# Performance work log

Measured on AMD Instinct MI355X. Metric: run time of the kernel, lower is better.

Reference implementation:

```python
import jax, jax.numpy as jnp
import numpy as np
from jax import lax

B, T, E, D = 32, 4096, 512, 512     # batch, x_steps, eunits, dunits
A, C, F = 128, 32, 15               # attn_dim, conv_channel, aconv_filts
K = 2 * F + 1                       # location conv kernel size
NEG = -1e9


def setup_inputs() -> dict:
    key = jax.random.key(0)
    ks = jax.random.split(key, 12)
    value = jax.random.normal(ks[0], (B, T, E), dtype=jnp.float32)
    value_length = jax.random.randint(ks[1], (B,), T // 2, T + 1).astype(jnp.int32)
    query = jax.random.normal(ks[2], (B, D), dtype=jnp.float32)
    # dirac initialization per initialize_weights()
    prev_attn_weight = jax.nn.one_hot(jnp.zeros((B,), jnp.int32), T, dtype=jnp.float32)
    accum_attn_weight = prev_attn_weight
    s = 0.02
    Wv = jax.random.normal(ks[3], (E, A), dtype=jnp.float32) * s
    bv = jnp.zeros((A,), jnp.float32)
    Wq = jax.random.normal(ks[4], (D, A), dtype=jnp.float32) * s
    conv_k = jax.random.normal(ks[5], (K, 1, C), dtype=jnp.float32) * s  # WIO
    Wl = jax.random.normal(ks[6], (C, A), dtype=jnp.float32) * s
    att_v = jax.random.normal(ks[7], (A,), dtype=jnp.float32)
    att_g = jnp.asarray(np.sqrt(1.0 / A), jnp.float32)
    att_b = jnp.zeros((A,), jnp.float32)
    score_bias = jnp.asarray(0.0, jnp.float32)
    return {"value": value, "value_length": value_length, "query": query,
            "accum_attn_weight": accum_attn_weight, "prev_attn_weight": prev_attn_weight,
            "Wv": Wv, "bv": bv, "Wq": Wq, "conv_k": conv_k, "Wl": Wl,
            "att_v": att_v, "att_g": att_g, "att_b": att_b, "score_bias": score_bias}


def _forward(value, value_length, query, accum_attn_weight, prev_attn_weight,
             Wv, bv, Wq, conv_k, Wl, att_v, att_g, att_b, score_bias):
    # projections
    densed_value = value @ Wv + bv                      # [B,T,A]
    densed_query = (query @ Wq)[:, None, :]             # [B,1,A]
    # location conv over accumulated weights, channels_last SAME
    loc = lax.conv_general_dilated(accum_attn_weight[:, :, None], conv_k,
                                   window_strides=(1,), padding='SAME',
                                   dimension_numbers=('NWC', 'WIO', 'NWC'))  # [B,T,C]
    attn_location = loc @ Wl                            # [B,T,A]
    # weight-normalized energy
    normed_v = att_g * att_v * lax.rsqrt(jnp.sum(jnp.square(att_v)))
    x = attn_location + densed_value + densed_query
    energy = jnp.einsum('bta,a->bt', jnp.tanh(x + att_b), normed_v) + score_bias
    mask = jnp.arange(T)[None, :] < value_length[:, None]
    energy = energy + (1.0 - mask.astype(energy.dtype)) * NEG
    # soft stepwise monotonic update (training=False: no sigmoid noise)
    p = jax.nn.sigmoid(energy)                          # [B,T]
    shifted = jnp.concatenate(
        [jnp.zeros((value.shape[0], 1), p.dtype),
         prev_attn_weight[:, :-1] * (1.0 - p[:, :-1])], axis=1)
    attn_weight = prev_attn_weight * p + shifted        # [B,T]
    attn_c = jnp.einsum('bt,bte->be', attn_weight, value)
    return attn_c, attn_weight


def reference(value, value_length, query, accum_attn_weight, prev_attn_weight,
              Wv, bv, Wq, conv_k, Wl, att_v, att_g, att_b, score_bias):
    return _forward(value, value_length, query, accum_attn_weight, prev_attn_weight,
                    Wv, bv, Wq, conv_k, Wl, att_v, att_g, att_b, score_bias)
```

## Files before the change

### kernel.cpp

```cpp
#include <hip/hip_runtime.h>
#include <hip/hip_bf16.h>

#define TT 4096
#define EE 512
#define AA 128

typedef short short8 __attribute__((ext_vector_type(8)));
typedef float f32x4 __attribute__((ext_vector_type(4)));

__device__ __forceinline__ short f2bf(float f) {
    union { float f; unsigned u; } v; v.f = f;
    unsigned r = v.u + 0x7fffu + ((v.u >> 16) & 1u);
    return (short)(r >> 16);
}
__device__ __forceinline__ unsigned pk2bf(float lo, float hi) {
    __hip_bfloat162 h = __float22bfloat162_rn(make_float2(lo, hi));
    union { __hip_bfloat162 h; unsigned u; } c; c.h = h;
    return c.u;
}

#define WS_WVT   0
#define WS_QBIAS 139264
#define WS_NV    155648
#define WS_P     156160
#define WS_PART  680448

__global__ void prep_kernel(const float* __restrict__ Wv, const float* __restrict__ conv_k,
                            const float* __restrict__ Wl, const float* __restrict__ query,
                            const float* __restrict__ Wq, const float* __restrict__ bv,
                            const float* __restrict__ att_b, const float* __restrict__ att_v,
                            const float* __restrict__ att_g,
                            short* __restrict__ wvt, float* __restrict__ q_bias,
                            float* __restrict__ nv) {
    if (blockIdx.x < 272) {
        int idx = blockIdx.x * 256 + threadIdx.x;
        int a = idx / 544, k = idx % 544;
        float val = 0.f;
        if (k < 512) {
            val = Wv[k * 128 + a];
        } else if (k < 543) {
            int kk = k - 512;
            float s = 0.f;
            #pragma unroll
            for (int c = 0; c < 32; ++c) s += conv_k[kk * 32 + c] * Wl[c * 128 + a];
            val = s;
        }
        wvt[a * 544 + k] = f2bf(val);
    } else {
        __shared__ float tmp[2][128];
        int b = blockIdx.x - 272;
        int a = threadIdx.x & 127, h = threadIdx.x >> 7;
        const float* q = query + b * 512 + h * 256;
        const float* wq = Wq + (h * 256) * 128 + a;
        float s = 0.f;
        #pragma unroll 4
        for (int d = 0; d < 256; ++d) s += q[d] * wq[d * 128];
        tmp[h][a] = s;
        __syncthreads();
        if (threadIdx.x < 128) {
            q_bias[b * 128 + a] = tmp[0][a] + tmp[1][a] + bv[a] + att_b[a];
            if (b == 0) {
                float ss = 0.f;
                #pragma unroll
                for (int i = 0; i < 128; ++i) { float t = att_v[i]; ss += t * t; }
                nv[a] = att_g[0] * att_v[a] * rsqrtf(ss);
            }
        }
    }
}

__global__ __launch_bounds__(256, 3) void energy_kernel(
    const float* __restrict__ value, const int* __restrict__ vlen,
    const float* __restrict__ accum, const short* __restrict__ wvt,
    const float* __restrict__ q_bias, const float* __restrict__ nv,
    const float* __restrict__ score_bias, float* __restrict__ p_buf) {

    __shared__ __align__(16) short As[2][128 * 40];
    __shared__ __align__(16) short Bs[2][128 * 40];

    int bid = blockIdx.x;
    int b  = bid >> 5;
    int t0 = (bid & 31) << 7;
    int tid = threadIdx.x;
    int w = tid >> 6;
    int l = tid & 63;
    int l15 = l & 15, g = l >> 4;

    int len = vlen[b];
    if (t0 >= len) {
        if (tid < 128) p_buf[b * TT + t0 + tid] = 0.f;
        return;
    }

    int arow[4], agrn[4];
    const float* abase[4];
    #pragma unroll
    for (int i = 0; i < 4; ++i) {
        int fl = tid + 256 * i;
        arow[i] = fl >> 3; agrn[i] = fl & 7;
        abase[i] = value + ((size_t)(b * TT + t0 + arow[i])) * EE + agrn[i] * 4;
    }
    int ba = tid >> 1, bh = (tid & 1) * 16;
    const short* bbase = wvt + ba * 544 + bh;

    f32x4 acc[2][8];
    #pragma unroll
    for (int rt = 0; rt < 2; ++rt)
        #pragma unroll
        for (int i = 0; i < 8; ++i) acc[rt][i] = (f32x4){0.f, 0.f, 0.f, 0.f};

    float4 av[4];
    short8 bv0, bv1;
    #pragma unroll
    for (int i = 0; i < 4; ++i) av[i] = *(const float4*)(abase[i]);
    bv0 = *(const short8*)(bbase);
    bv1 = *(const short8*)(bbase + 8);

    int cur = 0;
    for (int kc = 0; kc < 16; ++kc) {
        #pragma unroll
        for (int i = 0; i < 4; ++i) {
            uint2 pk;
            pk.x = pk2bf(av[i].x, av[i].y);
            pk.y = pk2bf(av[i].z, av[i].w);
            *(uint2*)(&As[cur][arow[i] * 40 + agrn[i] * 4]) = pk;
        }
        *(short8*)(&Bs[cur][ba * 40 + bh])     = bv0;
        *(short8*)(&Bs[cur][ba * 40 + bh + 8]) = bv1;

        if (kc < 15) {
            #pragma unroll
            for (int i = 0; i < 4; ++i) av[i] = *(const float4*)(abase[i] + (kc + 1) * 32);
            bv0 = *(const short8*)(bbase + (kc + 1) * 32);
            bv1 = *(const short8*)(bbase + (kc + 1) * 32 + 8);
        }
        __syncthreads();

        #pragma unroll
        for (int rt = 0; rt < 2; ++rt) {
            short8 af = *(const short8*)(&As[cur][(w * 32 + rt * 16 + l15) * 40 + g * 8]);
            #pragma unroll
            for (int t8 = 0; t8 < 8; ++t8) {
                short8 bf = *(const short8*)(&Bs[cur][(t8 * 16 + l15) * 40 + g * 8]);
                acc[rt][t8] = __builtin_amdgcn_mfma_f32_16x16x32_bf16(af, bf, acc[rt][t8], 0, 0, 0);
            }
        }
        cur ^= 1;
        __syncthreads();
    }

    #pragma unroll
    for (int rt = 0; rt < 2; ++rt) {
        int row = t0 + w * 32 + rt * 16 + l15;
        short8 af;
        #pragma unroll
        for (int i = 0; i < 8; ++i) {
            int kk = g * 8 + i;
            int t = row - 15 + kk;
            float v = (kk < 31 && t >= 0 && t < TT) ? accum[b * TT + t] : 0.f;
            af[i] = f2bf(v);
        }
        #pragma unroll
        for (int t8 = 0; t8 < 8; ++t8) {
            short8 bf = *(const short8*)(wvt + (t8 * 16 + l15) * 544 + 512 + g * 8);
            acc[rt][t8] = __builtin_amdgcn_mfma_f32_16x16x32_bf16(af, bf, acc[rt][t8], 0, 0, 0);
        }
    }

    float qb[8], nvv[8];
    #pragma unroll
    for (int t8 = 0; t8 < 8; ++t8) {
        int a = t8 * 16 + l15;
        qb[t8]  = q_bias[b * 128 + a];
        nvv[t8] = nv[a];
    }
    float sb = score_bias[0];
    #pragma unroll
    for (int rt = 0; rt < 2; ++rt) {
        #pragma unroll
        for (int j = 0; j < 4; ++j) {
            float e = 0.f;
            #pragma unroll
            for (int t8 = 0; t8 < 8; ++t8)
                e += tanhf(acc[rt][t8][j] + qb[t8]) * nvv[t8];
            e += __shfl_xor(e, 1);
            e += __shfl_xor(e, 2);
            e += __shfl_xor(e, 4);
            e += __shfl_xor(e, 8);
            if (l15 == 0) {
                int t = t0 + w * 32 + rt * 16 + g * 4 + j;
                float p = 0.f;
                if (t < len) { float ee = e + sb; p = 1.f / (1.f + expf(-ee)); }
                p_buf[b * TT + t] = p;
            }
        }
    }
}

__global__ __launch_bounds__(256) void ctx_fused(const float* __restrict__ value,
                                                 const float* __restrict__ p_buf,
                                                 const float* __restrict__ prev,
                                                 float* __restrict__ outw,
                                                 float* __restrict__ part) {
    __shared__ float wsm[512];
    __shared__ int flags[8];
    int b = blockIdx.x, tc = blockIdx.y;
    int tid = threadIdx.x;
    if (tid < 8) flags[tid] = 0;
    __syncthreads();

    int tl = tid * 2;
    {
        int t = tc * 512 + tl;
        int gi = b * TT + t;
        float w0 = prev[gi] * p_buf[gi];
        if (t > 0) w0 += prev[gi - 1] * (1.f - p_buf[gi - 1]);
        float w1 = prev[gi + 1] * p_buf[gi + 1] + prev[gi] * (1.f - p_buf[gi]);
        outw[gi] = w0; outw[gi + 1] = w1;
        wsm[tl] = w0; wsm[tl + 1] = w1;
        if (w0 != 0.f) flags[tl >> 6] = 1;
        if (w1 != 0.f) flags[(tl + 1) >> 6] = 1;
    }
    __syncthreads();

    float ax = 0.f, ay = 0.f;
    const float* vbase = value + ((size_t)b * TT + tc * 512) * EE + tid * 2;
    for (int c = 0; c < 8; ++c) {
        if (flags[c]) {
            #pragma unroll 4
            for (int tt = c * 64; tt < c * 64 + 64; ++tt) {
                float wv = wsm[tt];
                if (wv != 0.f) {
                    float2 v = *(const float2*)(vbase + (size_t)tt * EE);
                    ax += wv * v.x; ay += wv * v.y;
                }
            }
        }
    }
    float2 r; r.x = ax; r.y = ay;
    *(float2*)(part + ((b * 8 + tc) * 512) + tid * 2) = r;
}

__global__ void ctx_reduce(const float* __restrict__ part, float* __restrict__ outc) {
    int idx = blockIdx.x * 256 + threadIdx.x;
    int b = idx >> 9, e = idx & 511;
    float s = 0.f;
    #pragma unroll
    for (int tc = 0; tc < 8; ++tc) s += part[(b * 8 + tc) * 512 + e];
    outc[idx] = s;
}

extern "C" void kernel_launch(void* const* d_in, const int* in_sizes, int n_in,
                              void* d_out, int out_size, void* d_ws, size_t ws_size,
                              hipStream_t stream) {
    const float* value  = (const float*)d_in[0];
    const int*   vlen   = (const int*)  d_in[1];
    const float* query  = (const float*)d_in[2];
    const float* accum  = (const float*)d_in[3];
    const float* prev   = (const float*)d_in[4];
    const float* Wv     = (const float*)d_in[5];
    const float* bv     = (const float*)d_in[6];
    const float* Wq     = (const float*)d_in[7];
    const float* conv_k = (const float*)d_in[8];
    const float* Wl     = (const float*)d_in[9];
    const float* att_v  = (const float*)d_in[10];
    const float* att_g  = (const float*)d_in[11];
    const float* att_b  = (const float*)d_in[12];
    const float* sbias  = (const float*)d_in[13];

    char* wsb = (char*)d_ws;
    short* wvt   = (short*)(wsb + WS_WVT);
    float* qbias = (float*)(wsb + WS_QBIAS);
    float* nv    = (float*)(wsb + WS_NV);
    float* pbuf  = (float*)(wsb + WS_P);
    float* part  = (float*)(wsb + WS_PART);

    float* outc = (float*)d_out;
    float* outw = (float*)d_out + 32 * 512;

    prep_kernel<<<304, 256, 0, stream>>>(Wv, conv_k, Wl, query, Wq, bv, att_b,
                                         att_v, att_g, wvt, qbias, nv);
    energy_kernel<<<1024, 256, 0, stream>>>(value, vlen, accum, wvt, qbias, nv, sbias, pbuf);
    ctx_fused<<<dim3(32, 8), 256, 0, stream>>>(value, pbuf, prev, outw, part);
    ctx_reduce <<<64, 256, 0, stream>>>(part, outc);
}
```

Baseline: 424.4 us.

## Retile energy GEMM to 2x2 warp grid with 4x4 MFMA tiles and unrolled double buffer

The energy kernel's warp layout changes from each warp owning 32 rows by all 128 columns to a 2x2 warp grid where each warp owns 64 rows by 64 columns. Each k-step now loads 4 A and 4 B fragments per warp instead of 2 A and 16 B, which cuts shared-memory reads per MFMA. The main loop is manually unrolled by two with explicit ping-pong buffers, and the global loads for the next chunk are issued before compute. Because the energy reduction is now split across two column warps, partial sums go through a small shared array and one extra barrier before the sigmoid.

```diff
diff --git a/kernel.cpp b/kernel.cpp
--- a/kernel.cpp
+++ b/kernel.cpp
@@ -3,7 +3,6 @@
 
 #define TT 4096
 #define EE 512
-#define AA 128
 
 typedef short short8 __attribute__((ext_vector_type(8)));
 typedef float f32x4 __attribute__((ext_vector_type(4)));
@@ -77,13 +76,14 @@
 
     __shared__ __align__(16) short As[2][128 * 40];
     __shared__ __align__(16) short Bs[2][128 * 40];
+    __shared__ float esum[128][2];
 
     int bid = blockIdx.x;
     int b  = bid >> 5;
     int t0 = (bid & 31) << 7;
     int tid = threadIdx.x;
-    int w = tid >> 6;
-    int l = tid & 63;
+    int w = tid >> 6, l = tid & 63;
+    int wr = w >> 1, wc = w & 1;
     int l15 = l & 15, g = l >> 4;
 
     int len = vlen[b];
@@ -92,109 +92,127 @@
         return;
     }
 
-    int arow[4], agrn[4];
+    int arw[4], agr[4];
     const float* abase[4];
     #pragma unroll
     for (int i = 0; i < 4; ++i) {
         int fl = tid + 256 * i;
-        arow[i] = fl >> 3; agrn[i] = fl & 7;
-        abase[i] = value + ((size_t)(b * TT + t0 + arow[i])) * EE + agrn[i] * 4;
+        arw[i] = fl >> 3; agr[i] = fl & 7;
+        abase[i] = value + ((size_t)(b * TT + t0 + arw[i])) * EE + agr[i] * 4;
     }
     int ba = tid >> 1, bh = (tid & 1) * 16;
     const short* bbase = wvt + ba * 544 + bh;
 
-    f32x4 acc[2][8];
-    #pragma unroll
-    for (int rt = 0; rt < 2; ++rt)
+    f32x4 acc[4][4];
+    #pragma unroll
+    for (int i = 0; i < 4; ++i)
         #pragma unroll
-        for (int i = 0; i < 8; ++i) acc[rt][i] = (f32x4){0.f, 0.f, 0.f, 0.f};
-
-    float4 av[4];
-    short8 bv0, bv1;
-    #pragma unroll
-    for (int i = 0; i < 4; ++i) av[i] = *(const float4*)(abase[i]);
-    bv0 = *(const short8*)(bbase);
-    bv1 = *(const short8*)(bbase + 8);
-
-    int cur = 0;
-    for (int kc = 0; kc < 16; ++kc) {
+        for (int j = 0; j < 4; ++j) acc[i][j] = (f32x4){0.f, 0.f, 0.f, 0.f};
+
+#define LOAD_A(dst, kc) { _Pragma("unroll") \
+    for (int i = 0; i < 4; ++i) dst[i] = *(const float4*)(abase[i] + (kc) * 32); }
+#define LOAD_B(d0, d1, kc) { d0 = *(const short8*)(bbase + (kc) * 32); \
+                             d1 = *(const short8*)(bbase + (kc) * 32 + 8); }
+#define WRITE_BUF(bf_, av, b0, b1) { _Pragma("unroll") \
+    for (int i = 0; i < 4; ++i) { uint2 pk; \
+        pk.x = pk2bf(av[i].x, av[i].y); pk.y = pk2bf(av[i].z, av[i].w); \
+        *(uint2*)(&As[bf_][arw[i] * 40 + agr[i] * 4]) = pk; } \
+    *(short8*)(&Bs[bf_][ba * 40 + bh])     = b0; \
+    *(short8*)(&Bs[bf_][ba * 40 + bh + 8]) = b1; }
+#define COMPUTE(bf_) { short8 af[4], bq[4]; _Pragma("unroll") \
+    for (int rt = 0; rt < 4; ++rt) \
+        af[rt] = *(const short8*)(&As[bf_][(wr * 64 + rt * 16 + l15) * 40 + g * 8]); \
+    _Pragma("unroll") \
+    for (int ct = 0; ct < 4; ++ct) \
+        bq[ct] = *(const short8*)(&Bs[bf_][(wc * 64 + ct * 16 + l15) * 40 + g * 8]); \
+    _Pragma("unroll") \
+    for (int rt = 0; rt < 4; ++rt) \
+        _Pragma("unroll") \
+        for (int ct = 0; ct < 4; ++ct) \
+            acc[rt][ct] = __builtin_amdgcn_mfma_f32_16x16x32_bf16(af[rt], bq[ct], acc[rt][ct], 0, 0, 0); }
+
+    float4 avA[4], avB[4];
+    short8 bvA0, bvA1, bvB0, bvB1;
+
+    LOAD_A(avA, 0); LOAD_B(bvA0, bvA1, 0);
+    WRITE_BUF(0, avA, bvA0, bvA1);
+    LOAD_A(avB, 1); LOAD_B(bvB0, bvB1, 1);
+    __syncthreads();
+
+    for (int it = 0; it < 7; ++it) {
+        WRITE_BUF(1, avB, bvB0, bvB1);
+        LOAD_A(avA, 2 * it + 2); LOAD_B(bvA0, bvA1, 2 * it + 2);
+        COMPUTE(0);
+        __syncthreads();
+        WRITE_BUF(0, avA, bvA0, bvA1);
+        LOAD_A(avB, 2 * it + 3); LOAD_B(bvB0, bvB1, 2 * it + 3);
+        COMPUTE(1);
+        __syncthreads();
+    }
+    WRITE_BUF(1, avB, bvB0, bvB1);
+    COMPUTE(0);
+    __syncthreads();
+    COMPUTE(1);
+
+    {
+        short8 bq[4];
         #pragma unroll
-        for (int i = 0; i < 4; ++i) {
-            uint2 pk;
-            pk.x = pk2bf(av[i].x, av[i].y);
-            pk.y = pk2bf(av[i].z, av[i].w);
-            *(uint2*)(&As[cur][arow[i] * 40 + agrn[i] * 4]) = pk;
-        }
-        *(short8*)(&Bs[cur][ba * 40 + bh])     = bv0;
-        *(short8*)(&Bs[cur][ba * 40 + bh + 8]) = bv1;
-
-        if (kc < 15) {
+        for (int ct = 0; ct < 4; ++ct)
+            bq[ct] = *(const short8*)(wvt + (wc * 64 + ct * 16 + l15) * 544 + 512 + g * 8);
+        #pragma unroll
+        for (int rt = 0; rt < 4; ++rt) {
+            int row = t0 + wr * 64 + rt * 16 + l15;
+            short8 af;
             #pragma unroll
-            for (int i = 0; i < 4; ++i) av[i] = *(const float4*)(abase[i] + (kc + 1) * 32);
-            bv0 = *(const short8*)(bbase + (kc + 1) * 32);
-            bv1 = *(const short8*)(bbase + (kc + 1) * 32 + 8);
-        }
-        __syncthreads();
-
-        #pragma unroll
-        for (int rt = 0; rt < 2; ++rt) {
-            short8 af = *(const short8*)(&As[cur][(w * 32 + rt * 16 + l15) * 40 + g * 8]);
+            for (int i = 0; i < 8; ++i) {
+                int kk = g * 8 + i;
+                int t = row - 15 + kk;
+                float v = (kk < 31 && t >= 0 && t < TT) ? accum[b * TT + t] : 0.f;
+                af[i] = f2bf(v);
+            }
             #pragma unroll
-            for (int t8 = 0; t8 < 8; ++t8) {
-                short8 bf = *(const short8*)(&Bs[cur][(t8 * 16 + l15) * 40 + g * 8]);
-                acc[rt][t8] = __builtin_amdgcn_mfma_f32_16x16x32_bf16(af, bf, acc[rt][t8], 0, 0, 0);
-            }
-        }
-        cur ^= 1;
-        __syncthreads();
-    }
-
-    #pragma unroll
-    for (int rt = 0; rt < 2; ++rt) {
-        int row = t0 + w * 32 + rt * 16 + l15;
-        short8 af;
-        #pragma unroll
-        for (int i = 0; i < 8; ++i) {
-            int kk = g * 8 + i;
-            int t = row - 15 + kk;
-            float v = (kk < 31 && t >= 0 && t < TT) ? accum[b * TT + t] : 0.f;
-            af[i] = f2bf(v);
-        }
-        #pragma unroll
-        for (int t8 = 0; t8 < 8; ++t8) {
-            short8 bf = *(const short8*)(wvt + (t8 * 16 + l15) * 544 + 512 + g * 8);
-            acc[rt][t8] = __builtin_amdgcn_mfma_f32_16x16x32_bf16(af, bf, acc[rt][t8], 0, 0, 0);
-        }
-    }
-
-    float qb[8], nvv[8];
-    #pragma unroll
-    for (int t8 = 0; t8 < 8; ++t8) {
-        int a = t8 * 16 + l15;
-        qb[t8]  = q_bias[b * 128 + a];
-        nvv[t8] = nv[a];
-    }
-    float sb = score_bias[0];
-    #pragma unroll
-    for (int rt = 0; rt < 2; ++rt) {
+            for (int ct = 0; ct < 4; ++ct)
+                acc[rt][ct] = __builtin_amdgcn_mfma_f32_16x16x32_bf16(af, bq[ct], acc[rt][ct], 0, 0, 0);
+        }
+    }
+
+    float qb[4], nvv[4];
+    #pragma unroll
+    for (int ct = 0; ct < 4; ++ct) {
+        int a = wc * 64 + ct * 16 + l15;
+        qb[ct]  = q_bias[b * 128 + a];
+        nvv[ct] = nv[a];
+    }
+    __syncthreads();
+    #pragma unroll
+    for (int rt = 0; rt < 4; ++rt) {
         #pragma unroll
         for (int j = 0; j < 4; ++j) {
             float e = 0.f;
             #pragma unroll
-            for (int t8 = 0; t8 < 8; ++t8)
-                e += tanhf(acc[rt][t8][j] + qb[t8]) * nvv[t8];
+            for (int ct = 0; ct < 4; ++ct)
+                e += tanhf(acc[rt][ct][j] + qb[ct]) * nvv[ct];
             e += __shfl_xor(e, 1);
             e += __shfl_xor(e, 2);
             e += __shfl_xor(e, 4);
             e += __shfl_xor(e, 8);
-            if (l15 == 0) {
-                int t = t0 + w * 32 + rt * 16 + g * 4 + j;
-                float p = 0.f;
-                if (t < len) { float ee = e + sb; p = 1.f / (1.f + expf(-ee)); }
-                p_buf[b * TT + t] = p;
-            }
-        }
-    }
+            if (l15 == 0) esum[wr * 64 + rt * 16 + g * 4 + j][wc] = e;
+        }
+    }
+    __syncthreads();
+    if (tid < 128) {
+        int t = t0 + tid;
+        float p = 0.f;
+        if (t < len) {
+            float ee = esum[tid][0] + esum[tid][1] + score_bias[0];
+            p = 1.f / (1.f + expf(-ee));
+        }
+        p_buf[b * TT + t] = p;
+    }
+#undef LOAD_A
+#undef LOAD_B
+#undef WRITE_BUF
+#undef COMPUTE
 }
 
 __global__ __launch_bounds__(256) void ctx_fused(const float* __restrict__ value,
```

Result: slower. 433.2 us (+2.1%).
